# Performance work log

Measured on AMD Instinct MI355X. Metric: run time of the kernel, lower is better.

## Reference

```python
import jax, jax.numpy as jnp
import numpy as np

GRID_MIN, GRID_MAX, NUM_GRIDS = -2.0, 2.0, 15
DENOM = (GRID_MAX - GRID_MIN) / (NUM_GRIDS - 1)
LN_EPS = 1e-3  # tf.keras LayerNormalization default epsilon


def setup_inputs() -> dict:
    key = jax.random.key(0)
    k_x, k_sw, k_bw = jax.random.split(key, 3)
    N, D = 32768, 512
    G = NUM_GRIDS
    x = jax.random.normal(k_x, (N, D), dtype=jnp.float32)
    ln_gamma = jnp.ones((D,), dtype=jnp.float32)
    ln_beta = jnp.zeros((D,), dtype=jnp.float32)
    # Glorot-ish scaling to keep outputs sane
    spline_w = jax.random.normal(k_sw, (D, D * G), dtype=jnp.float32) * (1.0 / np.sqrt(D * G))
    base_w = jax.random.normal(k_bw, (D, D), dtype=jnp.float32) * (1.0 / np.sqrt(D))
    base_b = jnp.zeros((D,), dtype=jnp.float32)
    return {"x": x, "ln_gamma": ln_gamma, "ln_beta": ln_beta,
            "spline_w": spline_w, "base_w": base_w, "base_b": base_b}


def reference(x, ln_gamma, ln_beta, spline_w, base_w, base_b):
    N, D = x.shape
    G = NUM_GRIDS
    grid = jnp.linspace(GRID_MIN, GRID_MAX, G).astype(x.dtype)  # non-trainable buffer
    # LayerNorm over last axis (Keras: eps=1e-3)
    mean = jnp.mean(x, axis=-1, keepdims=True)
    var = jnp.mean(jnp.square(x - mean), axis=-1, keepdims=True)
    xn = (x - mean) * jax.lax.rsqrt(var + LN_EPS) * ln_gamma + ln_beta
    # RBF expansion: [N, D, G]
    basis = jnp.exp(-jnp.square((xn[..., None] - grid) / DENOM))
    # Spline GEMM: weight (out, D*G), y = basis_flat @ W^T
    w3 = spline_w.reshape(D, D, G)  # (out, in, grid)
    ret = jnp.einsum('ndg,odg->no', basis, w3)
    # Base residual: Dense(relu(x))
    base = jax.nn.relu(x) @ base_w + base_b
    return ret + base
```

## Files before the change

### kernel.cpp

```cpp
#include <hip/hip_runtime.h>
#include <hip/hip_bf16.h>
#include <stdint.h>

typedef __attribute__((ext_vector_type(8))) short short8;
typedef __attribute__((ext_vector_type(4))) float f32x4;
typedef __attribute__((ext_vector_type(4))) unsigned int u32x4;

#define NROWS 32768
#define DIM 512
#define KTOT 8192
#define KSPL 7680
#define LNEPS 1e-3f
#define SQL 4.20392843f

#if __has_builtin(__builtin_amdgcn_exp2f)
#define EXP2F(x) __builtin_amdgcn_exp2f(x)
#else
#define EXP2F(x) exp2f(x)
#endif

__device__ __forceinline__ unsigned short f2bf(float f) {
    unsigned u = __float_as_uint(f);
    u += 0x7fffu + ((u >> 16) & 1u);
    return (unsigned short)(u >> 16);
}

__device__ __forceinline__ unsigned pack_bf2(float a, float b) {
    unsigned ua = __float_as_uint(a) + 0x8000u;
    unsigned ub = __float_as_uint(b) + 0x8000u;
    return __builtin_amdgcn_perm(ub, ua, 0x07060302u);
}

__global__ __launch_bounds__(256) void prep_w_k(const float* __restrict__ sw,
                                                const float* __restrict__ bwt,
                                                unsigned short* __restrict__ Bw) {
    __shared__ float lds[KSPL];
    const int o = blockIdx.x;
    const int t = threadIdx.x;
    const float* swr = sw + (size_t)o * KSPL;
    unsigned short* br = Bw + (size_t)o * KTOT;
    #pragma unroll
    for (int it = 0; it < 30; ++it) lds[it * 256 + t] = swr[it * 256 + t];
    #pragma unroll
    for (int it = 0; it < 2; ++it) {
        int d = it * 256 + t;
        br[KSPL + d] = f2bf(bwt[(size_t)d * DIM + o]);
    }
    __syncthreads();
    #pragma unroll
    for (int it = 0; it < 30; ++it) {
        int k = it * 256 + t;
        int g = k >> 9, d = k & 511;
        br[k] = f2bf(lds[d * 15 + g]);
    }
}

__global__ __launch_bounds__(1024, 4) void kan_gemm(
    const float* __restrict__ x,
    const unsigned short* __restrict__ Bw,
    const float* __restrict__ gam,
    const float* __restrict__ bet,
    const float* __restrict__ bb,
    float* __restrict__ out) {
    __shared__ __align__(16) short As[128 * 64];
    __shared__ __align__(16) short Bs[512 * 64];

    const int t = threadIdx.x;
    const int w = t >> 6, l = t & 63;
    const int n0 = blockIdx.x << 7;

    const int ar  = t >> 3;
    const int kkg = t & 7;
    const int wm = (w >> 3) << 6;
    const int wn = (w & 7) << 6;
    const int fm = l & 15, fq = l >> 4;
    const int brow = l >> 3;
    const int bxor = (l & 7) ^ brow;
    const int asto = ((ar << 3) | (kkg ^ (ar & 7))) << 3;

    const float* xrow = x + (size_t)(n0 + ar) * DIM;
    float s = 0.f, ss = 0.f;
    #pragma unroll
    for (int it = 0; it < 16; ++it) {
        float4 v = *(const float4*)(xrow + it * 32 + ((t & 7) << 2));
        s  += v.x + v.y + v.z + v.w;
        ss += v.x * v.x + v.y * v.y + v.z * v.z + v.w * v.w;
    }
    #pragma unroll
    for (int m = 4; m >= 1; m >>= 1) {
        s  += __shfl_xor(s,  m, 64);
        ss += __shfl_xor(ss, m, 64);
    }
    const float mean = s * (1.0f / DIM);
    const float rstd = rsqrtf(ss * (1.0f / DIM) - mean * mean + LNEPS);
    const float sr = SQL * rstd;

    f32x4 acc[4][4];
    #pragma unroll
    for (int i = 0; i < 4; ++i)
        #pragma unroll
        for (int j = 0; j < 4; ++j)
            acc[i][j] = (f32x4)0.0f;

    #pragma unroll 1
    for (int dsb = 0; dsb < 8; ++dsb) {
        const int d0 = dsb << 6;
        const int dc = d0 + (kkg << 3);
        float xr[8], q[8];
        {
            float4 a = *(const float4*)(xrow + dc);
            float4 b = *(const float4*)(xrow + dc + 4);
            xr[0] = a.x; xr[1] = a.y; xr[2] = a.z; xr[3] = a.w;
            xr[4] = b.x; xr[5] = b.y; xr[6] = b.z; xr[7] = b.w;
            float4 g0 = *(const float4*)(gam + dc);
            float4 g1 = *(const float4*)(gam + dc + 4);
            float4 b0 = *(const float4*)(bet + dc);
            float4 b1 = *(const float4*)(bet + dc + 4);
            float gv[8] = {g0.x, g0.y, g0.z, g0.w, g1.x, g1.y, g1.z, g1.w};
            float bv[8] = {b0.x, b0.y, b0.z, b0.w, b1.x, b1.y, b1.z, b1.w};
            #pragma unroll
            for (int j = 0; j < 8; ++j) {
                float c = sr * gv[j];
                float o = __builtin_fmaf(-mean, c, SQL * bv[j]);
                q[j] = __builtin_fmaf(xr[j], c, o);
            }
        }
        #pragma unroll 1
        for (int g = 0; g < 16; ++g) {
            const int kc = (g < 15) ? ((g << 9) + d0) : (KSPL + d0);
            #pragma unroll
            for (int i = 0; i < 4; ++i) {
                const int rb = (i << 7) + (w << 3);
                const unsigned short* gp =
                    Bw + (size_t)(rb + brow) * KTOT + kc + (bxor << 3);
                __builtin_amdgcn_global_load_lds(
                    (const __attribute__((address_space(1))) void*)gp,
                    (__attribute__((address_space(3))) void*)&Bs[rb << 6],
                    16, 0, 0);
            }
            u32x4 v;
            if (g < 15) {
                const float qg = SQL * (-2.0f + (float)g * (2.0f / 7.0f));
                float e[8];
                #pragma unroll
                for (int j = 0; j < 8; ++j) {
                    float d = q[j] - qg;
                    e[j] = EXP2F(-(d * d));
                }
                v[0] = pack_bf2(e[0], e[1]);
                v[1] = pack_bf2(e[2], e[3]);
                v[2] = pack_bf2(e[4], e[5]);
                v[3] = pack_bf2(e[6], e[7]);
            } else {
                v[0] = pack_bf2(fmaxf(xr[0], 0.f), fmaxf(xr[1], 0.f));
                v[1] = pack_bf2(fmaxf(xr[2], 0.f), fmaxf(xr[3], 0.f));
                v[2] = pack_bf2(fmaxf(xr[4], 0.f), fmaxf(xr[5], 0.f));
                v[3] = pack_bf2(fmaxf(xr[6], 0.f), fmaxf(xr[7], 0.f));
            }
            *(u32x4*)&As[asto] = v;
            __syncthreads();
            #pragma unroll
            for (int ks = 0; ks < 2; ++ks) {
                const int kg = (ks << 2) + fq;
                short8 af[4], bfr[4];
                #pragma unroll
                for (int mt = 0; mt < 4; ++mt) {
                    const int m = wm + (mt << 4) + fm;
                    af[mt] = *(const short8*)&As[((m << 3) | (kg ^ (m & 7))) << 3];
                }
                #pragma unroll
                for (int nt = 0; nt < 4; ++nt) {
                    const int n = wn + (nt << 4) + fm;
                    bfr[nt] = *(const short8*)&Bs[((n << 3) | (kg ^ (n & 7))) << 3];
                }
                #pragma unroll
                for (int mt = 0; mt < 4; ++mt)
                    #pragma unroll
                    for (int nt = 0; nt < 4; ++nt)
                        acc[mt][nt] = __builtin_amdgcn_mfma_f32_16x16x32_bf16(
                            af[mt], bfr[nt], acc[mt][nt], 0, 0, 0);
            }
            __syncthreads();
        }
    }
    const int rq = fq << 2;
    float bias[4];
    #pragma unroll
    for (int nt = 0; nt < 4; ++nt) bias[nt] = bb[wn + (nt << 4) + fm];
    #pragma unroll
    for (int mt = 0; mt < 4; ++mt) {
        #pragma unroll
        for (int nt = 0; nt < 4; ++nt) {
            const int gr = n0 + wm + (mt << 4) + rq;
            const int gc = wn + (nt << 4) + fm;
            #pragma unroll
            for (int r = 0; r < 4; ++r)
                out[(size_t)(gr + r) * DIM + gc] = acc[mt][nt][r] + bias[nt];
        }
    }
}

extern "C" void kernel_launch(void* const* d_in, const int* in_sizes, int n_in,
                              void* d_out, int out_size, void* d_ws, size_t ws_size,
                              hipStream_t stream) {
    const float* x   = (const float*)d_in[0];
    const float* gam = (const float*)d_in[1];
    const float* bet = (const float*)d_in[2];
    const float* sw  = (const float*)d_in[3];
    const float* bwt = (const float*)d_in[4];
    const float* bb  = (const float*)d_in[5];
    float* out = (float*)d_out;

    unsigned short* Bw = (unsigned short*)d_ws;

    prep_w_k<<<dim3(512), dim3(256), 0, stream>>>(sw, bwt, Bw);
    kan_gemm<<<dim3(256), dim3(1024), 0, stream>>>(x, Bw, gam, bet, bb, out);
}
```

Measured before the change: 385.6 us.

## Double-buffer A/B LDS tiles and prefetch next B tile during MFMA

Both LDS tiles become ping-pong buffers. The global_load_lds for the next K-step's weight tile is issued right after the barrier, so it overlaps with the current MFMA work. This also removes the trailing barrier in each K iteration. In exchange, LDS use doubles to about 160KB per block, which uses the full LDS capacity, and correctness now depends on the async LDS loads being waited on before the next barrier.

```diff
diff --git a/kernel.cpp b/kernel.cpp
--- a/kernel.cpp
+++ b/kernel.cpp
@@ -62,8 +62,8 @@
     const float* __restrict__ bet,
     const float* __restrict__ bb,
     float* __restrict__ out) {
-    __shared__ __align__(16) short As[128 * 64];
-    __shared__ __align__(16) short Bs[512 * 64];
+    __shared__ __align__(16) short As[2][128 * 64];
+    __shared__ __align__(16) short Bs[2][512 * 64];
 
     const int t = threadIdx.x;
     const int w = t >> 6, l = t & 63;
@@ -101,6 +101,16 @@
         #pragma unroll
         for (int j = 0; j < 4; ++j)
             acc[i][j] = (f32x4)0.0f;
+
+    #pragma unroll
+    for (int i = 0; i < 4; ++i) {
+        const int rb = (i << 7) + (w << 3);
+        const unsigned short* gp = Bw + (size_t)(rb + brow) * KTOT + (bxor << 3);
+        __builtin_amdgcn_global_load_lds(
+            (const __attribute__((address_space(1))) void*)gp,
+            (__attribute__((address_space(3))) void*)&Bs[0][rb << 6],
+            16, 0, 0);
+    }
 
     #pragma unroll 1
     for (int dsb = 0; dsb < 8; ++dsb) {
@@ -125,19 +135,9 @@
                 q[j] = __builtin_fmaf(xr[j], c, o);
             }
         }
-        #pragma unroll 1
+        #pragma unroll 2
         for (int g = 0; g < 16; ++g) {
-            const int kc = (g < 15) ? ((g << 9) + d0) : (KSPL + d0);
-            #pragma unroll
-            for (int i = 0; i < 4; ++i) {
-                const int rb = (i << 7) + (w << 3);
-                const unsigned short* gp =
-                    Bw + (size_t)(rb + brow) * KTOT + kc + (bxor << 3);
-                __builtin_amdgcn_global_load_lds(
-                    (const __attribute__((address_space(1))) void*)gp,
-                    (__attribute__((address_space(3))) void*)&Bs[rb << 6],
-                    16, 0, 0);
-            }
+            const int p = g & 1;
             u32x4 v;
             if (g < 15) {
                 const float qg = SQL * (-2.0f + (float)g * (2.0f / 7.0f));
@@ -157,8 +157,26 @@
                 v[2] = pack_bf2(fmaxf(xr[4], 0.f), fmaxf(xr[5], 0.f));
                 v[3] = pack_bf2(fmaxf(xr[6], 0.f), fmaxf(xr[7], 0.f));
             }
-            *(u32x4*)&As[asto] = v;
+            *(u32x4*)&As[p][asto] = v;
             __syncthreads();
+            {
+                int gn = g + 1, dn = dsb;
+                if (gn == 16) { gn = 0; dn = dsb + 1; }
+                if (dn < 8) {
+                    const int kcn = (gn < 15) ? ((gn << 9) + (dn << 6))
+                                              : (KSPL + (dn << 6));
+                    #pragma unroll
+                    for (int i = 0; i < 4; ++i) {
+                        const int rb = (i << 7) + (w << 3);
+                        const unsigned short* gp =
+                            Bw + (size_t)(rb + brow) * KTOT + kcn + (bxor << 3);
+                        __builtin_amdgcn_global_load_lds(
+                            (const __attribute__((address_space(1))) void*)gp,
+                            (__attribute__((address_space(3))) void*)&Bs[p ^ 1][rb << 6],
+                            16, 0, 0);
+                    }
+                }
+            }
             #pragma unroll
             for (int ks = 0; ks < 2; ++ks) {
                 const int kg = (ks << 2) + fq;
@@ -166,12 +184,12 @@
                 #pragma unroll
                 for (int mt = 0; mt < 4; ++mt) {
                     const int m = wm + (mt << 4) + fm;
-                    af[mt] = *(const short8*)&As[((m << 3) | (kg ^ (m & 7))) << 3];
+                    af[mt] = *(const short8*)&As[p][((m << 3) | (kg ^ (m & 7))) << 3];
                 }
                 #pragma unroll
                 for (int nt = 0; nt < 4; ++nt) {
                     const int n = wn + (nt << 4) + fm;
-                    bfr[nt] = *(const short8*)&Bs[((n << 3) | (kg ^ (n & 7))) << 3];
+                    bfr[nt] = *(const short8*)&Bs[p][((n << 3) | (kg ^ (n & 7))) << 3];
                 }
                 #pragma unroll
                 for (int mt = 0; mt < 4; ++mt)
@@ -180,7 +198,6 @@
                         acc[mt][nt] = __builtin_amdgcn_mfma_f32_16x16x32_bf16(
                             af[mt], bfr[nt], acc[mt][nt], 0, 0, 0);
             }
-            __syncthreads();
         }
     }
     const int rq = fq << 2;
```

New measurement: 545.0 us. +41.3%, slower.
